# Performance work log

Measured on AMD Instinct MI355X. Metric: run time of the kernel, lower is better.

The kernel has to match this reference:

```python
import jax, jax.numpy as jnp
import numpy as np

# --- tree topology: complete binary tree, C = 2^(D+1)-1 nodes ---
K = 2           # branching factor
DEPTH = 10      # levels 0..DEPTH
C = 2 ** (DEPTH + 1) - 1   # 2047 classes
L = 4           # n_labels
B = 512         # batch size

_PARENT = (np.arange(C) - 1) // K          # parent index; node 0 is root
# nodes at depth d: [k^d - 1, k^(d+1) - 1) for k=2 -> [2^d-1, 2^(d+1)-1)
_LEVELS = [np.arange(2 ** d - 1, 2 ** (d + 1) - 1) for d in range(DEPTH + 1)]


def setup_inputs() -> dict:
    key = jax.random.key(0)
    k1, k2 = jax.random.split(key)
    X = jax.random.normal(k1, (B, C, L), dtype=jnp.float32)
    # torch.nn.init.uniform_(pairs, 0.1, 1.0)
    pairs = jax.random.uniform(k2, (C, C, L, L), dtype=jnp.float32,
                               minval=0.1, maxval=1.0)
    return {"X": X, "pairs": pairs}


def _upward(X, pairs):
    # alphas[b, i, y_i] = sum over children j of logsumexp_{y_j}(pairs[i,j,y_i,y_j] + X[b,j,y_j] + alphas[b,j,y_j])
    alphas = jnp.zeros((B, C, L), dtype=X.dtype)
    for d in range(DEPTH, 0, -1):          # leaves -> root (reversed BFS)
        nodes = _LEVELS[d]                 # children at this depth
        par = _PARENT[nodes]
        local = X[:, nodes, :] + alphas[:, nodes, :]        # (B, n, L_j)
        trans = pairs[par, nodes]                            # (n, L_i, L_j)
        msg = jax.nn.logsumexp(trans[None, :, :, :] + local[:, :, None, :], axis=-1)  # (B, n, L_i)
        alphas = alphas.at[:, par, :].add(msg)               # duplicate parents accumulate
    return alphas


def _downward(X, pairs):
    # betas[b, i, y_i] = logsumexp_{y_j}(pairs[i,j,y_i,y_j] + X[b,j,y_j] + betas[b,j,y_j]), j = parent(i)
    betas = jnp.zeros((B, C, L), dtype=X.dtype)
    for d in range(1, DEPTH + 1):          # root -> leaves (BFS)
        nodes = _LEVELS[d]                 # children receiving messages
        par = _PARENT[nodes]
        local = X[:, par, :] + betas[:, par, :]              # (B, n, L_j)
        trans = pairs[nodes, par]                            # (n, L_i, L_j): child-first index
        msg = jax.nn.logsumexp(trans[None, :, :, :] + local[:, :, None, :], axis=-1)
        betas = betas.at[:, nodes, :].add(msg)
    return betas


def reference(X, pairs):
    alphas = _upward(X, pairs)
    betas = _downward(X, pairs)
    logits = X + alphas + betas
    return jax.nn.log_softmax(logits, axis=-1)   # logits - logsumexp over labels
```

## Files before the change

kernel.cpp:

```cpp
#include <hip/hip_runtime.h>
#include <cstddef>

namespace {

constexpr int B     = 512;
constexpr int C     = 2047;
constexpr int L     = 4;
constexpr int DEPTH = 10;
constexpr int BLOCK = 512;
constexpr int NINT  = 1023;

__device__ __forceinline__ float4 ld4(const float* p) {
    return *reinterpret_cast<const float4*>(p);
}
__device__ __forceinline__ void st4(float* p, float x, float y, float z, float w) {
    float4 v; v.x = x; v.y = y; v.z = z; v.w = w;
    *reinterpret_cast<float4*>(p) = v;
}

__device__ __forceinline__ float lse4(float v0, float v1, float v2, float v3) {
    const float m = fmaxf(fmaxf(v0, v1), fmaxf(v2, v3));
    const float s = __expf(v0 - m) + __expf(v1 - m) + __expf(v2 - m) + __expf(v3 - m);
    return m + __logf(s);
}

__device__ __forceinline__ float4 msg4(const float* __restrict__ t,
                                       float l0, float l1, float l2, float l3) {
    const float4 t0 = ld4(t + 0);
    const float4 t1 = ld4(t + 4);
    const float4 t2 = ld4(t + 8);
    const float4 t3 = ld4(t + 12);
    float4 r;
    r.x = lse4(t0.x + l0, t0.y + l1, t0.z + l2, t0.w + l3);
    r.y = lse4(t1.x + l0, t1.y + l1, t1.z + l2, t1.w + l3);
    r.z = lse4(t2.x + l0, t2.y + l1, t2.z + l2, t2.w + l3);
    r.w = lse4(t3.x + l0, t3.y + l1, t3.z + l2, t3.w + l3);
    return r;
}

__device__ __forceinline__ void write_lsm(float* __restrict__ o,
                                          float g0, float g1, float g2, float g3) {
    const float z = lse4(g0, g1, g2, g3);
    st4(o, g0 - z, g1 - z, g2 - z, g3 - z);
}

__global__ __launch_bounds__(BLOCK, 4) void treecrf_kernel(
    const float* __restrict__ X,
    const float* __restrict__ pairs,
    float* __restrict__ out)
{
    __shared__ float alphas[NINT * L];
    __shared__ float fbo[512 * L];
    __shared__ float fbe[256 * L];

    const int b   = blockIdx.x;
    const int tid = threadIdx.x;
    const float* __restrict__ Xb = X + (size_t)b * (C * L);
    float* __restrict__ Ob       = out + (size_t)b * (C * L);

    {
        const int p  = 511 + tid;
        const int c0 = 2 * p + 1;
        const float4 x0 = ld4(Xb + c0 * L);
        const float4 x1 = ld4(Xb + (c0 + 1) * L);
        const float4 m0 = msg4(pairs + ((size_t)p * C + c0) * 16,
                               x0.x, x0.y, x0.z, x0.w);
        const float4 m1 = msg4(pairs + ((size_t)p * C + c0 + 1) * 16,
                               x1.x, x1.y, x1.z, x1.w);
        st4(&alphas[p * L], m0.x + m1.x, m0.y + m1.y, m0.z + m1.z, m0.w + m1.w);
    }
    __syncthreads();

    for (int d = 9; d >= 1; --d) {
        const int pn    = 1 << (d - 1);
        const int pbase = pn - 1;
        if (tid < pn) {
            const int p  = pbase + tid;
            const int c0 = 2 * p + 1;
            const float4 x0 = ld4(Xb + c0 * L);
            const float4 a0 = ld4(&alphas[c0 * L]);
            const float4 x1 = ld4(Xb + (c0 + 1) * L);
            const float4 a1 = ld4(&alphas[(c0 + 1) * L]);
            const float4 m0 = msg4(pairs + ((size_t)p * C + c0) * 16,
                                   x0.x + a0.x, x0.y + a0.y, x0.z + a0.z, x0.w + a0.w);
            const float4 m1 = msg4(pairs + ((size_t)p * C + c0 + 1) * 16,
                                   x1.x + a1.x, x1.y + a1.y, x1.z + a1.z, x1.w + a1.w);
            st4(&alphas[p * L], m0.x + m1.x, m0.y + m1.y, m0.z + m1.z, m0.w + m1.w);
        }
        __syncthreads();
    }

    if (tid < 2) {
        const int c = 1 + tid;
        const float4 x0 = ld4(Xb);
        const float4 m  = msg4(pairs + (size_t)c * C * 16,
                               x0.x, x0.y, x0.z, x0.w);
        st4(&fbo[(c - 1) * L], m.x, m.y, m.z, m.w);
        const float4 xc = ld4(Xb + c * L);
        const float4 ac = ld4(&alphas[c * L]);
        write_lsm(Ob + c * L, xc.x + ac.x + m.x, xc.y + ac.y + m.y,
                              xc.z + ac.z + m.z, xc.w + ac.w + m.w);
    } else if (tid == 2) {
        const float4 x0 = ld4(Xb);
        const float4 a0 = ld4(&alphas[0]);
        write_lsm(Ob, x0.x + a0.x, x0.y + a0.y, x0.z + a0.z, x0.w + a0.w);
    }
    __syncthreads();

    for (int d = 2; d <= DEPTH; ++d) {
        const int n     = 1 << d;
        const int base  = n - 1;
        const int pbase = (1 << (d - 1)) - 1;
        float* __restrict__ pbuf = ((d - 1) & 1) ? fbo : fbe;
        float* __restrict__ cbuf = (d & 1) ? fbo : fbe;
        for (int idx = tid; idx < n; idx += BLOCK) {
            const int c = base + idx;
            const int p = (c - 1) >> 1;
            const float4 xp = ld4(Xb + p * L);
            const float4 bp = ld4(&pbuf[(p - pbase) * L]);
            const float4 m  = msg4(pairs + ((size_t)c * C + p) * 16,
                                   xp.x + bp.x, xp.y + bp.y, xp.z + bp.z, xp.w + bp.w);
            if (d < DEPTH) st4(&cbuf[idx * L], m.x, m.y, m.z, m.w);
            const float4 xc = ld4(Xb + c * L);
            float a0 = 0.f, a1 = 0.f, a2 = 0.f, a3 = 0.f;
            if (d <= 9) {
                const float4 ac = ld4(&alphas[c * L]);
                a0 = ac.x; a1 = ac.y; a2 = ac.z; a3 = ac.w;
            }
            write_lsm(Ob + c * L, xc.x + a0 + m.x, xc.y + a1 + m.y,
                                  xc.z + a2 + m.z, xc.w + a3 + m.w);
        }
        if (d < DEPTH) __syncthreads();
    }
}

}

extern "C" void kernel_launch(void* const* d_in, const int* in_sizes, int n_in,
                              void* d_out, int out_size, void* d_ws, size_t ws_size,
                              hipStream_t stream) {
    (void)in_sizes; (void)n_in; (void)out_size; (void)d_ws; (void)ws_size;
    const float* X     = (const float*)d_in[0];
    const float* pairs = (const float*)d_in[1];
    float* out         = (float*)d_out;
    treecrf_kernel<<<B, BLOCK, 0, stream>>>(X, pairs, out);
}
```

Before: 36.09 us.

## Gather tree-edge transition matrices into compact coalesced workspace before main kernel

Adds a pre-pass kernel that copies only the 2046 parent/child transition blocks for each direction out of the huge pairs tensor into a compact, row-split workspace layout. The main kernel then reads these with coalesced float4 loads instead of scattered 64-byte blocks spread across a roughly 268MB array. It also folds the leaf level into the upward loop. The cost is an extra kernel launch plus the gather traffic, with a fallback path used when the workspace is too small.

Measured after the change: 38.37 us. 1.06x slower.

```diff
diff --git a/kernel.cpp b/kernel.cpp
--- a/kernel.cpp
+++ b/kernel.cpp
@@ -9,6 +9,11 @@
 constexpr int DEPTH = 10;
 constexpr int BLOCK = 512;
 constexpr int NINT  = 1023;
+
+constexpr int EDGES   = 2046;
+constexpr int ESTRIDE = 2048;
+constexpr size_t WS_F4   = 8 * (size_t)ESTRIDE;
+constexpr size_t WS_NEED = WS_F4 * 16;
 
 __device__ __forceinline__ float4 ld4(const float* p) {
     return *reinterpret_cast<const float4*>(p);
@@ -24,29 +29,39 @@
     return m + __logf(s);
 }
 
-__device__ __forceinline__ float4 msg4(const float* __restrict__ t,
-                                       float l0, float l1, float l2, float l3) {
-    const float4 t0 = ld4(t + 0);
-    const float4 t1 = ld4(t + 4);
-    const float4 t2 = ld4(t + 8);
-    const float4 t3 = ld4(t + 12);
-    float4 r;
-    r.x = lse4(t0.x + l0, t0.y + l1, t0.z + l2, t0.w + l3);
-    r.y = lse4(t1.x + l0, t1.y + l1, t1.z + l2, t1.w + l3);
-    r.z = lse4(t2.x + l0, t2.y + l1, t2.z + l2, t2.w + l3);
-    r.w = lse4(t3.x + l0, t3.y + l1, t3.z + l2, t3.w + l3);
-    return r;
-}
-
 __device__ __forceinline__ void write_lsm(float* __restrict__ o,
                                           float g0, float g1, float g2, float g3) {
     const float z = lse4(g0, g1, g2, g3);
     st4(o, g0 - z, g1 - z, g2 - z, g3 - z);
 }
 
+__global__ __launch_bounds__(256) void gather_pairs(
+    const float4* __restrict__ pairs4,
+    float4* __restrict__ ws)
+{
+    const int id  = blockIdx.x * 256 + threadIdx.x;
+    const int dir = id >> 13;
+    const int r   = (id >> 11) & 3;
+    const int e   = id & (ESTRIDE - 1);
+    if (e >= EDGES) return;
+    size_t src;
+    if (dir == 0) {
+        const int p = e >> 1;
+        const int c = 2 * p + 1 + (e & 1);
+        src = ((size_t)p * C + c) * 4 + r;
+    } else {
+        const int c = e + 1;
+        const int p = (c - 1) >> 1;
+        src = ((size_t)c * C + p) * 4 + r;
+    }
+    ws[(size_t)dir * (4 * ESTRIDE) + (size_t)r * ESTRIDE + e] = pairs4[src];
+}
+
+template <bool COMPACT>
 __global__ __launch_bounds__(BLOCK, 4) void treecrf_kernel(
     const float* __restrict__ X,
     const float* __restrict__ pairs,
+    const float4* __restrict__ cp,
     float* __restrict__ out)
 {
     __shared__ float alphas[NINT * L];
@@ -58,34 +73,38 @@
     const float* __restrict__ Xb = X + (size_t)b * (C * L);
     float* __restrict__ Ob       = out + (size_t)b * (C * L);
 
-    {
-        const int p  = 511 + tid;
-        const int c0 = 2 * p + 1;
-        const float4 x0 = ld4(Xb + c0 * L);
-        const float4 x1 = ld4(Xb + (c0 + 1) * L);
-        const float4 m0 = msg4(pairs + ((size_t)p * C + c0) * 16,
-                               x0.x, x0.y, x0.z, x0.w);
-        const float4 m1 = msg4(pairs + ((size_t)p * C + c0 + 1) * 16,
-                               x1.x, x1.y, x1.z, x1.w);
-        st4(&alphas[p * L], m0.x + m1.x, m0.y + m1.y, m0.z + m1.z, m0.w + m1.w);
-    }
-    __syncthreads();
-
-    for (int d = 9; d >= 1; --d) {
+    #pragma unroll 1
+    for (int d = DEPTH; d >= 1; --d) {
         const int pn    = 1 << (d - 1);
         const int pbase = pn - 1;
         if (tid < pn) {
             const int p  = pbase + tid;
             const int c0 = 2 * p + 1;
             const float4 x0 = ld4(Xb + c0 * L);
-            const float4 a0 = ld4(&alphas[c0 * L]);
             const float4 x1 = ld4(Xb + (c0 + 1) * L);
-            const float4 a1 = ld4(&alphas[(c0 + 1) * L]);
-            const float4 m0 = msg4(pairs + ((size_t)p * C + c0) * 16,
-                                   x0.x + a0.x, x0.y + a0.y, x0.z + a0.z, x0.w + a0.w);
-            const float4 m1 = msg4(pairs + ((size_t)p * C + c0 + 1) * 16,
-                                   x1.x + a1.x, x1.y + a1.y, x1.z + a1.z, x1.w + a1.w);
-            st4(&alphas[p * L], m0.x + m1.x, m0.y + m1.y, m0.z + m1.z, m0.w + m1.w);
+            float l00 = x0.x, l01 = x0.y, l02 = x0.z, l03 = x0.w;
+            float l10 = x1.x, l11 = x1.y, l12 = x1.z, l13 = x1.w;
+            if (d < DEPTH) {
+                const float4 a0 = ld4(&alphas[c0 * L]);
+                const float4 a1 = ld4(&alphas[(c0 + 1) * L]);
+                l00 += a0.x; l01 += a0.y; l02 += a0.z; l03 += a0.w;
+                l10 += a1.x; l11 += a1.y; l12 += a1.z; l13 += a1.w;
+            }
+            float acc[4];
+            #pragma unroll
+            for (int r = 0; r < 4; ++r) {
+                float4 t0, t1;
+                if (COMPACT) {
+                    t0 = cp[(size_t)r * ESTRIDE + 2 * p];
+                    t1 = cp[(size_t)r * ESTRIDE + 2 * p + 1];
+                } else {
+                    t0 = ld4(pairs + ((size_t)p * C + c0) * 16 + r * 4);
+                    t1 = ld4(pairs + ((size_t)p * C + c0 + 1) * 16 + r * 4);
+                }
+                acc[r] = lse4(t0.x + l00, t0.y + l01, t0.z + l02, t0.w + l03)
+                       + lse4(t1.x + l10, t1.y + l11, t1.z + l12, t1.w + l13);
+            }
+            st4(&alphas[p * L], acc[0], acc[1], acc[2], acc[3]);
         }
         __syncthreads();
     }
@@ -93,13 +112,19 @@
     if (tid < 2) {
         const int c = 1 + tid;
         const float4 x0 = ld4(Xb);
-        const float4 m  = msg4(pairs + (size_t)c * C * 16,
-                               x0.x, x0.y, x0.z, x0.w);
-        st4(&fbo[(c - 1) * L], m.x, m.y, m.z, m.w);
+        float m[4];
+        #pragma unroll
+        for (int r = 0; r < 4; ++r) {
+            const float4 t = COMPACT
+                ? cp[(size_t)(4 + r) * ESTRIDE + (c - 1)]
+                : ld4(pairs + (size_t)c * C * 16 + r * 4);
+            m[r] = lse4(t.x + x0.x, t.y + x0.y, t.z + x0.z, t.w + x0.w);
+        }
+        st4(&fbo[(c - 1) * L], m[0], m[1], m[2], m[3]);
         const float4 xc = ld4(Xb + c * L);
         const float4 ac = ld4(&alphas[c * L]);
-        write_lsm(Ob + c * L, xc.x + ac.x + m.x, xc.y + ac.y + m.y,
-                              xc.z + ac.z + m.z, xc.w + ac.w + m.w);
+        write_lsm(Ob + c * L, xc.x + ac.x + m[0], xc.y + ac.y + m[1],
+                              xc.z + ac.z + m[2], xc.w + ac.w + m[3]);
     } else if (tid == 2) {
         const float4 x0 = ld4(Xb);
         const float4 a0 = ld4(&alphas[0]);
@@ -107,6 +132,7 @@
     }
     __syncthreads();
 
+    #pragma unroll 1
     for (int d = 2; d <= DEPTH; ++d) {
         const int n     = 1 << d;
         const int base  = n - 1;
@@ -118,17 +144,25 @@
             const int p = (c - 1) >> 1;
             const float4 xp = ld4(Xb + p * L);
             const float4 bp = ld4(&pbuf[(p - pbase) * L]);
-            const float4 m  = msg4(pairs + ((size_t)c * C + p) * 16,
-                                   xp.x + bp.x, xp.y + bp.y, xp.z + bp.z, xp.w + bp.w);
-            if (d < DEPTH) st4(&cbuf[idx * L], m.x, m.y, m.z, m.w);
+            const float lp0 = xp.x + bp.x, lp1 = xp.y + bp.y;
+            const float lp2 = xp.z + bp.z, lp3 = xp.w + bp.w;
+            float m[4];
+            #pragma unroll
+            for (int r = 0; r < 4; ++r) {
+                const float4 t = COMPACT
+                    ? cp[(size_t)(4 + r) * ESTRIDE + (c - 1)]
+                    : ld4(pairs + ((size_t)c * C + p) * 16 + r * 4);
+                m[r] = lse4(t.x + lp0, t.y + lp1, t.z + lp2, t.w + lp3);
+            }
+            if (d < DEPTH) st4(&cbuf[idx * L], m[0], m[1], m[2], m[3]);
             const float4 xc = ld4(Xb + c * L);
             float a0 = 0.f, a1 = 0.f, a2 = 0.f, a3 = 0.f;
             if (d <= 9) {
                 const float4 ac = ld4(&alphas[c * L]);
                 a0 = ac.x; a1 = ac.y; a2 = ac.z; a3 = ac.w;
             }
-            write_lsm(Ob + c * L, xc.x + a0 + m.x, xc.y + a1 + m.y,
-                                  xc.z + a2 + m.z, xc.w + a3 + m.w);
+            write_lsm(Ob + c * L, xc.x + a0 + m[0], xc.y + a1 + m[1],
+                                  xc.z + a2 + m[2], xc.w + a3 + m[3]);
         }
         if (d < DEPTH) __syncthreads();
     }
@@ -139,9 +173,16 @@
 extern "C" void kernel_launch(void* const* d_in, const int* in_sizes, int n_in,
                               void* d_out, int out_size, void* d_ws, size_t ws_size,
                               hipStream_t stream) {
-    (void)in_sizes; (void)n_in; (void)out_size; (void)d_ws; (void)ws_size;
+    (void)in_sizes; (void)n_in; (void)out_size;
     const float* X     = (const float*)d_in[0];
     const float* pairs = (const float*)d_in[1];
     float* out         = (float*)d_out;
-    treecrf_kernel<<<B, BLOCK, 0, stream>>>(X, pairs, out);
+
+    if (ws_size >= WS_NEED) {
+        float4* ws = (float4*)d_ws;
+        gather_pairs<<<64, 256, 0, stream>>>((const float4*)pairs, ws);
+        treecrf_kernel<true><<<B, BLOCK, 0, stream>>>(X, pairs, ws, out);
+    } else {
+        treecrf_kernel<false><<<B, BLOCK, 0, stream>>>(X, pairs, nullptr, out);
+    }
 }
```

## Run narrow tree levels in a single wavefront with wave barriers, halve block size

Applied to the files above, without the earlier changes.

Levels with at most 64 nodes, both upward (parents 0..126) and downward (depths 2..6), now run inside one 64-lane wavefront. They sync with wave barriers instead of block-wide __syncthreads. The block shrinks from 512 to 256 threads, with wide levels unrolled into fixed per-thread loops, and the two child messages are fused into one helper. This is meant to cut block-level barrier latency on the serial depth chain and let more blocks share a CU. The cost is that intra-wave LDS ordering now rests on wave-barrier semantics, and threads 64..255 sit idle longer.

Result: faster. 34.59 us (-4.2%).

```diff
diff --git a/kernel.cpp b/kernel.cpp
--- a/kernel.cpp
+++ b/kernel.cpp
@@ -6,16 +6,18 @@
 constexpr int B     = 512;
 constexpr int C     = 2047;
 constexpr int L     = 4;
-constexpr int DEPTH = 10;
-constexpr int BLOCK = 512;
+constexpr int BLOCK = 256;
 constexpr int NINT  = 1023;
 
 __device__ __forceinline__ float4 ld4(const float* p) {
     return *reinterpret_cast<const float4*>(p);
 }
-__device__ __forceinline__ void st4(float* p, float x, float y, float z, float w) {
-    float4 v; v.x = x; v.y = y; v.z = z; v.w = w;
+__device__ __forceinline__ void st4f(float* p, const float4 v) {
     *reinterpret_cast<float4*>(p) = v;
+}
+__device__ __forceinline__ float4 add4(const float4 a, const float4 b) {
+    float4 r; r.x = a.x + b.x; r.y = a.y + b.y; r.z = a.z + b.z; r.w = a.w + b.w;
+    return r;
 }
 
 __device__ __forceinline__ float lse4(float v0, float v1, float v2, float v3) {
@@ -24,27 +26,53 @@
     return m + __logf(s);
 }
 
-__device__ __forceinline__ float4 msg4(const float* __restrict__ t,
-                                       float l0, float l1, float l2, float l3) {
-    const float4 t0 = ld4(t + 0);
-    const float4 t1 = ld4(t + 4);
-    const float4 t2 = ld4(t + 8);
-    const float4 t3 = ld4(t + 12);
-    float4 r;
-    r.x = lse4(t0.x + l0, t0.y + l1, t0.z + l2, t0.w + l3);
-    r.y = lse4(t1.x + l0, t1.y + l1, t1.z + l2, t1.w + l3);
-    r.z = lse4(t2.x + l0, t2.y + l1, t2.z + l2, t2.w + l3);
-    r.w = lse4(t3.x + l0, t3.y + l1, t3.z + l2, t3.w + l3);
-    return r;
-}
-
-__device__ __forceinline__ void write_lsm(float* __restrict__ o,
-                                          float g0, float g1, float g2, float g3) {
-    const float z = lse4(g0, g1, g2, g3);
-    st4(o, g0 - z, g1 - z, g2 - z, g3 - z);
-}
-
-__global__ __launch_bounds__(BLOCK, 4) void treecrf_kernel(
+__device__ __forceinline__ void write_lsm(float* __restrict__ o, const float4 g) {
+    const float z = lse4(g.x, g.y, g.z, g.w);
+    float4 r; r.x = g.x - z; r.y = g.y - z; r.z = g.z - z; r.w = g.w - z;
+    st4f(o, r);
+}
+
+__device__ __forceinline__ float4 up2(const float* __restrict__ pairs, int p,
+                                      const float4 lc0, const float4 lc1) {
+    const int c0 = 2 * p + 1;
+    const float* __restrict__ t = pairs + ((size_t)p * C + c0) * 16;
+    float4 acc;
+    {
+        const float4 a = ld4(t + 0), bq = ld4(t + 16);
+        acc.x = lse4(a.x + lc0.x, a.y + lc0.y, a.z + lc0.z, a.w + lc0.w)
+              + lse4(bq.x + lc1.x, bq.y + lc1.y, bq.z + lc1.z, bq.w + lc1.w);
+    }
+    {
+        const float4 a = ld4(t + 4), bq = ld4(t + 20);
+        acc.y = lse4(a.x + lc0.x, a.y + lc0.y, a.z + lc0.z, a.w + lc0.w)
+              + lse4(bq.x + lc1.x, bq.y + lc1.y, bq.z + lc1.z, bq.w + lc1.w);
+    }
+    {
+        const float4 a = ld4(t + 8), bq = ld4(t + 24);
+        acc.z = lse4(a.x + lc0.x, a.y + lc0.y, a.z + lc0.z, a.w + lc0.w)
+              + lse4(bq.x + lc1.x, bq.y + lc1.y, bq.z + lc1.z, bq.w + lc1.w);
+    }
+    {
+        const float4 a = ld4(t + 12), bq = ld4(t + 28);
+        acc.w = lse4(a.x + lc0.x, a.y + lc0.y, a.z + lc0.z, a.w + lc0.w)
+              + lse4(bq.x + lc1.x, bq.y + lc1.y, bq.z + lc1.z, bq.w + lc1.w);
+    }
+    return acc;
+}
+
+__device__ __forceinline__ float4 dn_msg(const float* __restrict__ pairs,
+                                         int c, int p, const float4 lp) {
+    const float* __restrict__ t = pairs + ((size_t)c * C + p) * 16;
+    const float4 t0 = ld4(t + 0), t1 = ld4(t + 4), t2 = ld4(t + 8), t3 = ld4(t + 12);
+    float4 m;
+    m.x = lse4(t0.x + lp.x, t0.y + lp.y, t0.z + lp.z, t0.w + lp.w);
+    m.y = lse4(t1.x + lp.x, t1.y + lp.y, t1.z + lp.z, t1.w + lp.w);
+    m.z = lse4(t2.x + lp.x, t2.y + lp.y, t2.z + lp.z, t2.w + lp.w);
+    m.w = lse4(t3.x + lp.x, t3.y + lp.y, t3.z + lp.z, t3.w + lp.w);
+    return m;
+}
+
+__global__ __launch_bounds__(BLOCK, 2) void treecrf_kernel(
     const float* __restrict__ X,
     const float* __restrict__ pairs,
     float* __restrict__ out)
@@ -52,6 +80,8 @@
     __shared__ float alphas[NINT * L];
     __shared__ float fbo[512 * L];
     __shared__ float fbe[256 * L];
+    __shared__ float fbA[32 * L];
+    __shared__ float fbB[64 * L];
 
     const int b   = blockIdx.x;
     const int tid = threadIdx.x;
@@ -59,78 +89,122 @@
     float* __restrict__ Ob       = out + (size_t)b * (C * L);
 
     {
-        const int p  = 511 + tid;
+        int p = 511 + tid;
+        const float4 l0 = ld4(Xb + (2 * p + 1) * L);
+        const float4 l1 = ld4(Xb + (2 * p + 2) * L);
+        int q = p + 256;
+        const float4 m0 = ld4(Xb + (2 * q + 1) * L);
+        const float4 m1 = ld4(Xb + (2 * q + 2) * L);
+        st4f(&alphas[p * L], up2(pairs, p, l0, l1));
+        st4f(&alphas[q * L], up2(pairs, q, m0, m1));
+    }
+    __syncthreads();
+
+    {
+        const int p  = 255 + tid;
         const int c0 = 2 * p + 1;
-        const float4 x0 = ld4(Xb + c0 * L);
-        const float4 x1 = ld4(Xb + (c0 + 1) * L);
-        const float4 m0 = msg4(pairs + ((size_t)p * C + c0) * 16,
-                               x0.x, x0.y, x0.z, x0.w);
-        const float4 m1 = msg4(pairs + ((size_t)p * C + c0 + 1) * 16,
-                               x1.x, x1.y, x1.z, x1.w);
-        st4(&alphas[p * L], m0.x + m1.x, m0.y + m1.y, m0.z + m1.z, m0.w + m1.w);
-    }
-    __syncthreads();
-
-    for (int d = 9; d >= 1; --d) {
-        const int pn    = 1 << (d - 1);
-        const int pbase = pn - 1;
-        if (tid < pn) {
-            const int p  = pbase + tid;
-            const int c0 = 2 * p + 1;
-            const float4 x0 = ld4(Xb + c0 * L);
-            const float4 a0 = ld4(&alphas[c0 * L]);
-            const float4 x1 = ld4(Xb + (c0 + 1) * L);
-            const float4 a1 = ld4(&alphas[(c0 + 1) * L]);
-            const float4 m0 = msg4(pairs + ((size_t)p * C + c0) * 16,
-                                   x0.x + a0.x, x0.y + a0.y, x0.z + a0.z, x0.w + a0.w);
-            const float4 m1 = msg4(pairs + ((size_t)p * C + c0 + 1) * 16,
-                                   x1.x + a1.x, x1.y + a1.y, x1.z + a1.z, x1.w + a1.w);
-            st4(&alphas[p * L], m0.x + m1.x, m0.y + m1.y, m0.z + m1.z, m0.w + m1.w);
-        }
-        __syncthreads();
-    }
-
-    if (tid < 2) {
-        const int c = 1 + tid;
+        const float4 l0 = add4(ld4(Xb + c0 * L), ld4(&alphas[c0 * L]));
+        const float4 l1 = add4(ld4(Xb + (c0 + 1) * L), ld4(&alphas[(c0 + 1) * L]));
+        st4f(&alphas[p * L], up2(pairs, p, l0, l1));
+    }
+    __syncthreads();
+
+    if (tid < 128) {
+        const int p  = 127 + tid;
+        const int c0 = 2 * p + 1;
+        const float4 l0 = add4(ld4(Xb + c0 * L), ld4(&alphas[c0 * L]));
+        const float4 l1 = add4(ld4(Xb + (c0 + 1) * L), ld4(&alphas[(c0 + 1) * L]));
+        st4f(&alphas[p * L], up2(pairs, p, l0, l1));
+    }
+    __syncthreads();
+
+    if (tid < 64) {
+        #pragma unroll 1
+        for (int pn = 64; pn >= 1; pn >>= 1) {
+            if (tid < pn) {
+                const int p  = pn - 1 + tid;
+                const int c0 = 2 * p + 1;
+                const float4 l0 = add4(ld4(Xb + c0 * L), ld4(&alphas[c0 * L]));
+                const float4 l1 = add4(ld4(Xb + (c0 + 1) * L), ld4(&alphas[(c0 + 1) * L]));
+                st4f(&alphas[p * L], up2(pairs, p, l0, l1));
+            }
+            __builtin_amdgcn_wave_barrier();
+        }
+
         const float4 x0 = ld4(Xb);
-        const float4 m  = msg4(pairs + (size_t)c * C * 16,
-                               x0.x, x0.y, x0.z, x0.w);
-        st4(&fbo[(c - 1) * L], m.x, m.y, m.z, m.w);
-        const float4 xc = ld4(Xb + c * L);
-        const float4 ac = ld4(&alphas[c * L]);
-        write_lsm(Ob + c * L, xc.x + ac.x + m.x, xc.y + ac.y + m.y,
-                              xc.z + ac.z + m.z, xc.w + ac.w + m.w);
-    } else if (tid == 2) {
-        const float4 x0 = ld4(Xb);
-        const float4 a0 = ld4(&alphas[0]);
-        write_lsm(Ob, x0.x + a0.x, x0.y + a0.y, x0.z + a0.z, x0.w + a0.w);
-    }
-    __syncthreads();
-
-    for (int d = 2; d <= DEPTH; ++d) {
-        const int n     = 1 << d;
-        const int base  = n - 1;
-        const int pbase = (1 << (d - 1)) - 1;
-        float* __restrict__ pbuf = ((d - 1) & 1) ? fbo : fbe;
-        float* __restrict__ cbuf = (d & 1) ? fbo : fbe;
-        for (int idx = tid; idx < n; idx += BLOCK) {
-            const int c = base + idx;
-            const int p = (c - 1) >> 1;
-            const float4 xp = ld4(Xb + p * L);
-            const float4 bp = ld4(&pbuf[(p - pbase) * L]);
-            const float4 m  = msg4(pairs + ((size_t)c * C + p) * 16,
-                                   xp.x + bp.x, xp.y + bp.y, xp.z + bp.z, xp.w + bp.w);
-            if (d < DEPTH) st4(&cbuf[idx * L], m.x, m.y, m.z, m.w);
-            const float4 xc = ld4(Xb + c * L);
-            float a0 = 0.f, a1 = 0.f, a2 = 0.f, a3 = 0.f;
-            if (d <= 9) {
-                const float4 ac = ld4(&alphas[c * L]);
-                a0 = ac.x; a1 = ac.y; a2 = ac.z; a3 = ac.w;
+        if (tid == 0) {
+            write_lsm(Ob, add4(x0, ld4(&alphas[0])));
+        }
+        if (tid < 2) {
+            const int c = 1 + tid;
+            const float4 m = dn_msg(pairs, c, 0, x0);
+            st4f(&fbA[tid * L], m);
+            write_lsm(Ob + c * L,
+                      add4(add4(ld4(Xb + c * L), ld4(&alphas[c * L])), m));
+        }
+        __builtin_amdgcn_wave_barrier();
+
+        #pragma unroll 1
+        for (int d = 2; d <= 6; ++d) {
+            const int n     = 1 << d;
+            const int base  = n - 1;
+            const int pbase = (1 << (d - 1)) - 1;
+            const float* __restrict__ pb = (d & 1) ? fbB : fbA;
+            float* __restrict__       cb = (d & 1) ? fbA : fbB;
+            if (tid < n) {
+                const int c = base + tid;
+                const int p = (c - 1) >> 1;
+                const float4 lp = add4(ld4(Xb + p * L), ld4(&pb[(p - pbase) * L]));
+                const float4 m  = dn_msg(pairs, c, p, lp);
+                st4f(&cb[tid * L], m);
+                write_lsm(Ob + c * L,
+                          add4(add4(ld4(Xb + c * L), ld4(&alphas[c * L])), m));
             }
-            write_lsm(Ob + c * L, xc.x + a0 + m.x, xc.y + a1 + m.y,
-                                  xc.z + a2 + m.z, xc.w + a3 + m.w);
-        }
-        if (d < DEPTH) __syncthreads();
+            __builtin_amdgcn_wave_barrier();
+        }
+    }
+    __syncthreads();
+
+    if (tid < 128) {
+        const int c = 127 + tid;
+        const int p = (c - 1) >> 1;
+        const float4 lp = add4(ld4(Xb + p * L), ld4(&fbB[(p - 63) * L]));
+        const float4 m  = dn_msg(pairs, c, p, lp);
+        st4f(&fbo[tid * L], m);
+        write_lsm(Ob + c * L, add4(add4(ld4(Xb + c * L), ld4(&alphas[c * L])), m));
+    }
+    __syncthreads();
+
+    {
+        const int c = 255 + tid;
+        const int p = (c - 1) >> 1;
+        const float4 lp = add4(ld4(Xb + p * L), ld4(&fbo[(p - 127) * L]));
+        const float4 m  = dn_msg(pairs, c, p, lp);
+        st4f(&fbe[tid * L], m);
+        write_lsm(Ob + c * L, add4(add4(ld4(Xb + c * L), ld4(&alphas[c * L])), m));
+    }
+    __syncthreads();
+
+    #pragma unroll
+    for (int k = 0; k < 2; ++k) {
+        const int idx = tid + k * 256;
+        const int c   = 511 + idx;
+        const int p   = (c - 1) >> 1;
+        const float4 lp = add4(ld4(Xb + p * L), ld4(&fbe[(p - 255) * L]));
+        const float4 m  = dn_msg(pairs, c, p, lp);
+        st4f(&fbo[idx * L], m);
+        write_lsm(Ob + c * L, add4(add4(ld4(Xb + c * L), ld4(&alphas[c * L])), m));
+    }
+    __syncthreads();
+
+    #pragma unroll
+    for (int k = 0; k < 4; ++k) {
+        const int idx = tid + k * 256;
+        const int c   = 1023 + idx;
+        const int p   = (c - 1) >> 1;
+        const float4 lp = add4(ld4(Xb + p * L), ld4(&fbo[(p - 511) * L]));
+        const float4 m  = dn_msg(pairs, c, p, lp);
+        write_lsm(Ob + c * L, add4(ld4(Xb + c * L), m));
     }
 }
 
```
